# Kernel optimization log

Measured on AMD Instinct MI355X. Metric: run time of the kernel, lower is better.

## Reference

```python
import jax, jax.numpy as jnp
import numpy as np

B, T, C = 2, 2048, 2048
N_HEAD, N_KV_HEAD = 16, 4
HEAD_DIM = C // N_HEAD  # 128
N_REP = N_HEAD // N_KV_HEAD  # 4


def setup_inputs() -> dict:
    key = jax.random.key(0)
    ks = jax.random.split(key, 5)
    x = jax.random.normal(ks[0], (B, T, C), dtype=jnp.float32)
    # RoPE freqs (theta=10000), real cos/sin form of torch's complex freqs_cis
    inv_freq = 1.0 / (10000.0 ** (jnp.arange(0, HEAD_DIM, 2, dtype=jnp.float32) / HEAD_DIM))
    angles = jnp.arange(T, dtype=jnp.float32)[:, None] * inv_freq[None, :]  # [T, HEAD_DIM//2]
    freqs_cos = jnp.cos(angles)
    freqs_sin = jnp.sin(angles)
    s = 0.02
    wq = jax.random.normal(ks[1], (C, C), dtype=jnp.float32) * s
    wk = jax.random.normal(ks[2], (N_KV_HEAD * HEAD_DIM, C), dtype=jnp.float32) * s
    wv = jax.random.normal(ks[3], (N_KV_HEAD * HEAD_DIM, C), dtype=jnp.float32) * s
    wo = jax.random.normal(ks[4], (C, C), dtype=jnp.float32) * s
    return {"x": x, "freqs_cos": freqs_cos, "freqs_sin": freqs_sin,
            "wq": wq, "wk": wk, "wv": wv, "wo": wo}


def _apply_rotary(t, cos, sin):
    # t: [B, T, H, D]; pairs (even, odd) treated as complex, multiplied by cos+i*sin
    tr = t.reshape(*t.shape[:-1], -1, 2)  # [B,T,H,D/2,2]
    t0, t1 = tr[..., 0], tr[..., 1]
    c = cos[None, :, None, :]  # [1,T,1,D/2]
    s = sin[None, :, None, :]
    out = jnp.stack([t0 * c - t1 * s, t0 * s + t1 * c], axis=-1)
    return out.reshape(t.shape)


def reference(x, freqs_cos, freqs_sin, wq, wk, wv, wo):
    b, t, _ = x.shape
    xq = (x @ wq.T).reshape(b, t, N_HEAD, HEAD_DIM)
    xk = (x @ wk.T).reshape(b, t, N_KV_HEAD, HEAD_DIM)
    xv = (x @ wv.T).reshape(b, t, N_KV_HEAD, HEAD_DIM)
    xq = _apply_rotary(xq, freqs_cos, freqs_sin)
    xk = _apply_rotary(xk, freqs_cos, freqs_sin)
    # GQA: repeat_interleave kv heads to n_head
    xk_r = jnp.repeat(xk, N_REP, axis=2)
    xv_r = jnp.repeat(xv, N_REP, axis=2)
    # [B,H,T,D]
    q = xq.transpose(0, 2, 1, 3)
    k = xk_r.transpose(0, 2, 1, 3)
    v = xv_r.transpose(0, 2, 1, 3)
    scale = 1.0 / jnp.sqrt(jnp.float32(HEAD_DIM))
    scores = jnp.einsum('bhtd,bhsd->bhts', q, k) * scale
    causal = jnp.tril(jnp.ones((t, t), dtype=bool))
    scores = jnp.where(causal[None, None], scores, jnp.finfo(scores.dtype).min)
    attn = jax.nn.softmax(scores, axis=-1)
    y = jnp.einsum('bhts,bhsd->bhtd', attn, v)
    y = y.transpose(0, 2, 1, 3).reshape(b, t, C)
    return y @ wo.T
```

## Files before the change

### kernel.cpp

```cpp
#include <hip/hip_runtime.h>

typedef __attribute__((ext_vector_type(8))) __bf16 bf16x8;
typedef __attribute__((ext_vector_type(4))) __bf16 bf16x4;
typedef __attribute__((ext_vector_type(4))) float floatx4;

#define MFMA16x16x32 __builtin_amdgcn_mfma_f32_16x16x32_bf16

__device__ __forceinline__ void async_load16(const void* g, void* l) {
  __builtin_amdgcn_global_load_lds((const __attribute__((address_space(1))) void*)g,
                                   (__attribute__((address_space(3))) void*)l, 16, 0, 0);
}

__global__ __launch_bounds__(256) void cast_all_kernel(const float* __restrict__ x,
                                                       const float* __restrict__ wq,
                                                       const float* __restrict__ wk,
                                                       const float* __restrict__ wv,
                                                       const float* __restrict__ wo,
                                                       __bf16* __restrict__ dst) {
  int i = blockIdx.x * blockDim.x + threadIdx.x;
  const float* src;
  int off;
  if (i < 2097152)      { src = x;  off = 0; }
  else if (i < 3145728) { src = wq; off = 2097152; }
  else if (i < 3407872) { src = wk; off = 3145728; }
  else if (i < 3670016) { src = wv; off = 3407872; }
  else                  { src = wo; off = 3670016; }
  float4 v = ((const float4*)src)[i - off];
  bf16x4 o;
  o[0] = (__bf16)v.x; o[1] = (__bf16)v.y; o[2] = (__bf16)v.z; o[3] = (__bf16)v.w;
  *(bf16x4*)(dst + (size_t)i * 4) = o;
}

template <int MODE>
__global__ __launch_bounds__(256, 3) void gemm_bt(const __bf16* __restrict__ A,
                                                  const __bf16* __restrict__ Bw,
                                                  float* __restrict__ C,
                                                  const float* __restrict__ cs,
                                                  const float* __restrict__ sn,
                                                  __bf16* __restrict__ qb,
                                                  __bf16* __restrict__ kb,
                                                  __bf16* __restrict__ vtg,
                                                  int M, int N, int K) {
  __shared__ __bf16 As[128][64];
  __shared__ __bf16 Bs[128][64];
  const int tid = threadIdx.x;
  const int wave = tid >> 6, lane = tid & 63;
  const int quad = lane >> 4, l16 = lane & 15;
  const int wm = (wave >> 1) * 64, wn = (wave & 1) * 64;
  const int row0 = blockIdx.y * 128, col0 = blockIdx.x * 128;
  const int lr = lane >> 3, ls = lane & 7;
  const int segg = ls ^ lr;
  floatx4 acc[4][4] = {};
  const __bf16* Ab = A + (size_t)row0 * K + segg * 8;
  const __bf16* Bb = Bw + (size_t)col0 * K + segg * 8;
  for (int k0 = 0; k0 < K; k0 += 64) {
    __syncthreads();
#pragma unroll
    for (int i = 0; i < 4; i++) {
      int c = wave * 4 + i;
      int r = c * 8 + lr;
      async_load16(Ab + (size_t)r * K + k0, &As[c * 8][0]);
      async_load16(Bb + (size_t)r * K + k0, &Bs[c * 8][0]);
    }
    __syncthreads();
#pragma unroll
    for (int kk = 0; kk < 64; kk += 32) {
      bf16x8 af[4], bfr[4];
#pragma unroll
      for (int mt = 0; mt < 4; mt++) {
        int row = wm + mt * 16 + l16;
        int seg = ((kk >> 3) + quad) ^ (row & 7);
        af[mt] = *(const bf16x8*)&As[row][seg * 8];
      }
#pragma unroll
      for (int nt = 0; nt < 4; nt++) {
        int row = wn + nt * 16 + l16;
        int seg = ((kk >> 3) + quad) ^ (row & 7);
        bfr[nt] = *(const bf16x8*)&Bs[row][seg * 8];
      }
#pragma unroll
      for (int mt = 0; mt < 4; mt++)
#pragma unroll
        for (int nt = 0; nt < 4; nt++)
          acc[mt][nt] = MFMA16x16x32(af[mt], bfr[nt], acc[mt][nt], 0, 0, 0);
    }
  }
  if (MODE == 0) {
#pragma unroll
    for (int mt = 0; mt < 4; mt++)
#pragma unroll
      for (int nt = 0; nt < 4; nt++)
#pragma unroll
        for (int r = 0; r < 4; r++) {
          int row = row0 + wm + mt * 16 + quad * 4 + r;
          int col = col0 + wn + nt * 16 + l16;
          C[(size_t)row * N + col] = acc[mt][nt][r];
        }
  } else {
#pragma unroll
    for (int mt = 0; mt < 4; mt++)
#pragma unroll
      for (int nt = 0; nt < 4; nt++) {
        const int cbase = col0 + wn + nt * 16;
        const int c = cbase + l16;
#pragma unroll
        for (int r = 0; r < 4; r++) {
          int row = row0 + wm + mt * 16 + quad * 4 + r;
          int t = row & 2047;
          float v = acc[mt][nt][r];
          float vp = __shfl_xor(v, 1);
          if (cbase < 2048) {
            int i = (c & 127) >> 1;
            float co = cs[t * 64 + i], si = sn[t * 64 + i];
            qb[(size_t)row * 2048 + c] =
                (__bf16)((v * co + ((c & 1) ? vp : -vp) * si) * 0.1275411391f);
          } else if (cbase < 2560) {
            int i = (c & 127) >> 1;
            float co = cs[t * 64 + i], si = sn[t * 64 + i];
            kb[(size_t)row * 512 + c - 2048] = (__bf16)(v * co + ((c & 1) ? vp : -vp) * si);
          } else {
            int vd = c - 2560;
            vtg[((size_t)(row >> 11) * 512 + vd) * 2048 + t] = (__bf16)v;
          }
        }
      }
  }
}

__global__ __launch_bounds__(256, 2) void attn_kernel(const __bf16* __restrict__ qb,
                                                      const __bf16* __restrict__ kb,
                                                      const __bf16* __restrict__ vtg,
                                                      __bf16* __restrict__ yb) {
  const int id = blockIdx.x;
  const int q1 = id >> 8;
  const int cc = id & 255;
  const int kvh = cc & 3;
  const int b = (cc >> 2) & 1;
  const int s5 = (cc >> 3) & 31;
  const int tile = q1 ? (63 - s5) : s5;
  const int tid = threadIdx.x, wave = tid >> 6, lane = tid & 63;
  const int h = kvh * 4 + wave;
  const int quad = lane >> 4, l16 = lane & 15;
  const int q0 = tile * 32;
  __shared__ __bf16 Ks[2][64][128];
  __shared__ __bf16 Vt[2][128][64];
  __shared__ __bf16 Ps[4][2][16][64];
  const __bf16* kbase = kb + (size_t)b * 2048 * 512 + kvh * 128;
  const __bf16* vbase = vtg + ((size_t)b * 512 + kvh * 128) * 2048;

  const int u16   = (quad ^ (l16 & 3)) * 16;
  const int b2_64 = (l16 & 4) ? 64 : 0;
  char* const ksb = (char*)Ks;
  char* const vtb = (char*)Vt;
  char* const psb = (char*)Ps + wave * 4096;
  char* const kA0 = ksb + l16 * 256 + u16 + b2_64;
  char* const kB0 = kA0 + 64 - 2 * b2_64;
  char* const kA1 = kA0 + 16384;
  char* const kB1 = kB0 + 16384;
  char* const vA0 = vtb + l16 * 128 + u16 + b2_64;
  char* const vB0 = vA0 + 64 - 2 * b2_64;
  char* const vA1 = vA0 + 16384;
  char* const vB1 = vB0 + 16384;
  char* const prA = psb + l16 * 128 + u16 + b2_64;
  char* const prB = prA + 64 - 2 * b2_64;
  const int h16 = (l16 & 8) ? 16 : 0;
  const int q64 = (quad & 1) * 64;
  char* const pw00 = psb + quad * 512 + (l16 & 7) * 2 + h16 + q64;
  char* const pw10 = psb + quad * 512 + (l16 & 7) * 2 + (16 - h16) + q64;
  char* const pw01 = pw00 + 64 - 2 * q64;
  char* const pw11 = pw10 + 64 - 2 * q64;

  const int klr4 = lane >> 4, kls = lane & 15;
  const int vlr8 = lane >> 3, vls = lane & 7;
  const __bf16* ksrc[4];
  const __bf16* vsrc[4];
#pragma unroll
  for (int i = 0; i < 4; i++) {
    int row = (wave * 4 + i) * 4 + klr4;
    ksrc[i] = kbase + (size_t)row * 512 + (kls ^ (row & 7)) * 8;
    int d = (wave * 4 + i) * 8 + vlr8;
    vsrc[i] = vbase + (size_t)d * 2048 + (vls ^ (d & 7)) * 8;
  }
  char* const kdst = ksb + wave * 4096;
  char* const vdst = vtb + wave * 4096;

  auto stage = [&](int pb, int s0) {
#pragma unroll
    for (int i = 0; i < 4; i++)
      async_load16(ksrc[i] + (size_t)s0 * 512, kdst + pb * 16384 + i * 1024);
#pragma unroll
    for (int i = 0; i < 4; i++)
      async_load16(vsrc[i] + s0, vdst + pb * 16384 + i * 1024);
  };

  bf16x8 qf[2][4];
#pragma unroll
  for (int mt = 0; mt < 2; mt++)
#pragma unroll
    for (int kc = 0; kc < 4; kc++)
      qf[mt][kc] = *(const bf16x8*)(qb + (size_t)(b * 2048 + q0 + mt * 16 + l16) * 2048 +
                                    h * 128 + kc * 32 + quad * 8);
  bf16x8 ones;
#pragma unroll
  for (int j = 0; j < 8; j++) ones[j] = (__bf16)1.0f;
  floatx4 o[2][8] = {};
  floatx4 lsum[2] = {};
  const int nblocks = (tile + 2) >> 1;

  stage(0, 0);
  __syncthreads();

  for (int it = 0; it < nblocks; it++) {
    const int cur = it & 1;
    const int s0 = it * 64;
    if (it + 1 < nblocks) stage(cur ^ 1, s0 + 64);
    const char* kA = cur ? kA1 : kA0;
    const char* kB = cur ? kB1 : kB0;
    const char* vA = cur ? vA1 : vA0;
    const char* vB = cur ? vB1 : vB0;
    floatx4 sacc[2][4] = {};
    __builtin_amdgcn_s_setprio(1);
#pragma unroll
    for (int kc = 0; kc < 4; kc++) {
      const char* kbp = (kc & 1) ? kB : kA;
      bf16x8 bfr[4];
#pragma unroll
      for (int nt = 0; nt < 4; nt++)
        bfr[nt] = *(const bf16x8*)(kbp + nt * 4096 + (kc >> 1) * 128);
#pragma unroll
      for (int mt = 0; mt < 2; mt++)
#pragma unroll
        for (int nt = 0; nt < 4; nt++)
          sacc[mt][nt] = MFMA16x16x32(qf[mt][kc], bfr[nt], sacc[mt][nt], 0, 0, 0);
    }
    __builtin_amdgcn_s_setprio(0);
    const bool diag = (it == nblocks - 1);
#pragma unroll
    for (int mt = 0; mt < 2; mt++)
#pragma unroll
      for (int r = 0; r < 4; r++) {
        const int qg = q0 + mt * 16 + quad * 4 + r;
#pragma unroll
        for (int nt = 0; nt < 4; nt++) {
          float p = __builtin_exp2f(sacc[mt][nt][r]);
          if (diag) { int keyg = s0 + nt * 16 + l16; p = (keyg <= qg) ? p : 0.f; }
          char* w = (r & 1) ? ((nt < 2) ? pw10 : pw11) : ((nt < 2) ? pw00 : pw01);
          *(__bf16*)(w + mt * 2048 + r * 128 + ((nt & 1) ^ (r >> 1)) * 32) = (__bf16)p;
        }
      }
    __builtin_amdgcn_s_setprio(1);
#pragma unroll
    for (int c2 = 0; c2 < 2; c2++) {
      const char* pr = c2 ? prB : prA;
      const char* vv = c2 ? vB : vA;
      bf16x8 pa[2];
#pragma unroll
      for (int mt = 0; mt < 2; mt++) {
        pa[mt] = *(const bf16x8*)(pr + mt * 2048);
        lsum[mt] = MFMA16x16x32(pa[mt], ones, lsum[mt], 0, 0, 0);
      }
#pragma unroll
      for (int dt = 0; dt < 8; dt++) {
        bf16x8 vf = *(const bf16x8*)(vv + dt * 2048);
#pragma unroll
        for (int mt = 0; mt < 2; mt++)
          o[mt][dt] = MFMA16x16x32(pa[mt], vf, o[mt][dt], 0, 0, 0);
      }
    }
    __builtin_amdgcn_s_setprio(0);
    __syncthreads();
  }
#pragma unroll
  for (int mt = 0; mt < 2; mt++) {
    float inv[4];
#pragma unroll
    for (int r = 0; r < 4; r++) inv[r] = 1.f / lsum[mt][r];
#pragma unroll
    for (int dt = 0; dt < 8; dt++)
#pragma unroll
      for (int r = 0; r < 4; r++) {
        int qg = q0 + mt * 16 + quad * 4 + r;
        yb[(size_t)(b * 2048 + qg) * 2048 + h * 128 + dt * 16 + l16] =
            (__bf16)(o[mt][dt][r] * inv[r]);
      }
  }
}

extern "C" void kernel_launch(void* const* d_in, const int* in_sizes, int n_in,
                              void* d_out, int out_size, void* d_ws, size_t ws_size,
                              hipStream_t stream) {
  const float* x  = (const float*)d_in[0];
  const float* fc = (const float*)d_in[1];
  const float* fs = (const float*)d_in[2];
  const float* wq = (const float*)d_in[3];
  const float* wk = (const float*)d_in[4];
  const float* wv = (const float*)d_in[5];
  const float* wo = (const float*)d_in[6];
  float* out = (float*)d_out;
  char* ws = (char*)d_ws;

  __bf16* xb   = (__bf16*)(ws);
  __bf16* wqkv = (__bf16*)(ws + 16777216);
  __bf16* wob  = (__bf16*)(ws + 29360128);
  __bf16* qbuf = (__bf16*)(ws + 37748736);
  __bf16* kbuf = (__bf16*)(ws + 54525952);
  __bf16* vtg  = (__bf16*)(ws + 58720256);
  __bf16* ybuf = (__bf16*)(ws + 62914560);

  cast_all_kernel<<<18432, 256, 0, stream>>>(x, wq, wk, wv, wo, xb);

  gemm_bt<1><<<dim3(24, 32), 256, 0, stream>>>(xb, wqkv, nullptr, fc, fs,
                                               qbuf, kbuf, vtg, 4096, 3072, 2048);

  attn_kernel<<<dim3(512), 256, 0, stream>>>(qbuf, kbuf, vtg, ybuf);

  gemm_bt<0><<<dim3(16, 32), 256, 0, stream>>>(ybuf, wob, out, nullptr, nullptr,
                                               nullptr, nullptr, nullptr, 4096, 2048, 2048);
}
```

Before: 304.2 us.

## Split long causal attention tiles across two blocks and stage V-transpose through LDS

```diff
diff --git a/kernel.cpp b/kernel.cpp
--- a/kernel.cpp
+++ b/kernel.cpp
@@ -102,49 +102,77 @@
 #pragma unroll
       for (int nt = 0; nt < 4; nt++) {
         const int cbase = col0 + wn + nt * 16;
-        const int c = cbase + l16;
-#pragma unroll
-        for (int r = 0; r < 4; r++) {
-          int row = row0 + wm + mt * 16 + quad * 4 + r;
-          int t = row & 2047;
-          float v = acc[mt][nt][r];
-          float vp = __shfl_xor(v, 1);
-          if (cbase < 2048) {
+        if (cbase < 2560) {
+          const int c = cbase + l16;
+#pragma unroll
+          for (int r = 0; r < 4; r++) {
+            int row = row0 + wm + mt * 16 + quad * 4 + r;
+            int t = row & 2047;
+            float v = acc[mt][nt][r];
+            float vp = __shfl_xor(v, 1);
             int i = (c & 127) >> 1;
             float co = cs[t * 64 + i], si = sn[t * 64 + i];
-            qb[(size_t)row * 2048 + c] =
-                (__bf16)((v * co + ((c & 1) ? vp : -vp) * si) * 0.1275411391f);
-          } else if (cbase < 2560) {
-            int i = (c & 127) >> 1;
-            float co = cs[t * 64 + i], si = sn[t * 64 + i];
-            kb[(size_t)row * 512 + c - 2048] = (__bf16)(v * co + ((c & 1) ? vp : -vp) * si);
-          } else {
-            int vd = c - 2560;
-            vtg[((size_t)(row >> 11) * 512 + vd) * 2048 + t] = (__bf16)v;
+            float rv = v * co + ((c & 1) ? vp : -vp) * si;
+            if (cbase < 2048) {
+              qb[(size_t)row * 2048 + c] = (__bf16)(rv * 0.1275411391f);
+            } else {
+              kb[(size_t)row * 512 + c - 2048] = (__bf16)rv;
+            }
           }
         }
       }
+    __syncthreads();
+    __bf16* Vl = &As[0][0] + wave * 1024;
+    const int brow = row0 + wm;
+#pragma unroll
+    for (int nt = 0; nt < 4; nt++) {
+      const int cbase = col0 + wn + nt * 16;
+      if (cbase >= 2560) {
+#pragma unroll
+        for (int mt = 0; mt < 4; mt++)
+#pragma unroll
+          for (int r = 0; r < 4; r++)
+            Vl[l16 * 64 + mt * 16 + quad * 4 + r] = (__bf16)acc[mt][nt][r];
+        asm volatile("" ::: "memory");
+        const int vB = cbase - 2560;
+#pragma unroll
+        for (int p = 0; p < 4; p++) {
+          int vdl = p * 4 + (lane >> 4);
+          int tl = (lane & 15) * 4;
+          bf16x4 val = *(const bf16x4*)&Vl[vdl * 64 + tl];
+          *(bf16x4*)&vtg[((size_t)(brow >> 11) * 512 + vB + vdl) * 2048 +
+                         (brow & 2047) + tl] = val;
+        }
+        asm volatile("" ::: "memory");
+      }
+    }
   }
 }
 
 __global__ __launch_bounds__(256, 2) void attn_kernel(const __bf16* __restrict__ qb,
                                                       const __bf16* __restrict__ kb,
                                                       const __bf16* __restrict__ vtg,
-                                                      __bf16* __restrict__ yb) {
+                                                      __bf16* __restrict__ yb,
+                                                      float* __restrict__ opart,
+                                                      float* __restrict__ lpart,
+                                                      int* __restrict__ ctr,
+                                                      int* __restrict__ ready) {
   const int id = blockIdx.x;
-  const int q1 = id >> 8;
-  const int cc = id & 255;
-  const int kvh = cc & 3;
-  const int b = (cc >> 2) & 1;
-  const int s5 = (cc >> 3) & 31;
-  const int tile = q1 ? (63 - s5) : s5;
+  int grp, tile, chunk, split;
+  if (id < 512) { grp = id >> 6; tile = 32 + ((id & 63) >> 1); chunk = id & 1; split = 1; }
+  else          { int k = id - 512; grp = k >> 5; tile = k & 31; chunk = 0; split = 0; }
+  const int kvh = grp & 3, b = grp >> 2;
   const int tid = threadIdx.x, wave = tid >> 6, lane = tid & 63;
   const int h = kvh * 4 + wave;
   const int quad = lane >> 4, l16 = lane & 15;
   const int q0 = tile * 32;
+  const int nb = (tile + 2) >> 1;
+  const int it0 = chunk * 16;
+  const int it1 = split ? (chunk ? nb : 16) : nb;
   __shared__ __bf16 Ks[2][64][128];
   __shared__ __bf16 Vt[2][128][64];
   __shared__ __bf16 Ps[4][2][16][64];
+  __shared__ int tk_sh;
   const __bf16* kbase = kb + (size_t)b * 2048 * 512 + kvh * 128;
   const __bf16* vbase = vtg + ((size_t)b * 512 + kvh * 128) * 2048;
 
@@ -205,15 +233,14 @@
   for (int j = 0; j < 8; j++) ones[j] = (__bf16)1.0f;
   floatx4 o[2][8] = {};
   floatx4 lsum[2] = {};
-  const int nblocks = (tile + 2) >> 1;
-
-  stage(0, 0);
+
+  stage(it0 & 1, it0 * 64);
   __syncthreads();
 
-  for (int it = 0; it < nblocks; it++) {
+  for (int it = it0; it < it1; it++) {
     const int cur = it & 1;
     const int s0 = it * 64;
-    if (it + 1 < nblocks) stage(cur ^ 1, s0 + 64);
+    if (it + 1 < it1) stage(cur ^ 1, s0 + 64);
     const char* kA = cur ? kA1 : kA0;
     const char* kB = cur ? kB1 : kB0;
     const char* vA = cur ? vA1 : vA0;
@@ -234,7 +261,7 @@
           sacc[mt][nt] = MFMA16x16x32(qf[mt][kc], bfr[nt], sacc[mt][nt], 0, 0, 0);
     }
     __builtin_amdgcn_s_setprio(0);
-    const bool diag = (it == nblocks - 1);
+    const bool diag = (it == nb - 1);
 #pragma unroll
     for (int mt = 0; mt < 2; mt++)
 #pragma unroll
@@ -270,19 +297,86 @@
     __builtin_amdgcn_s_setprio(0);
     __syncthreads();
   }
-#pragma unroll
-  for (int mt = 0; mt < 2; mt++) {
-    float inv[4];
-#pragma unroll
-    for (int r = 0; r < 4; r++) inv[r] = 1.f / lsum[mt][r];
-#pragma unroll
-    for (int dt = 0; dt < 8; dt++)
-#pragma unroll
-      for (int r = 0; r < 4; r++) {
-        int qg = q0 + mt * 16 + quad * 4 + r;
-        yb[(size_t)(b * 2048 + qg) * 2048 + h * 128 + dt * 16 + l16] =
-            (__bf16)(o[mt][dt][r] * inv[r]);
-      }
+
+  if (!split) {
+#pragma unroll
+    for (int mt = 0; mt < 2; mt++) {
+      float inv[4];
+#pragma unroll
+      for (int r = 0; r < 4; r++) inv[r] = 1.f / lsum[mt][r];
+#pragma unroll
+      for (int dt = 0; dt < 8; dt++)
+#pragma unroll
+        for (int r = 0; r < 4; r++) {
+          int qg = q0 + mt * 16 + quad * 4 + r;
+          yb[(size_t)(b * 2048 + qg) * 2048 + h * 128 + dt * 16 + l16] =
+              (__bf16)(o[mt][dt][r] * inv[r]);
+        }
+    }
+  } else {
+    const int pair = grp * 32 + (tile - 32);
+    float* oslot = opart + (size_t)pair * 16384;
+    float* lslot = lpart + (size_t)pair * 128;
+    if (tid == 0)
+      tk_sh = __hip_atomic_fetch_add(&ctr[pair], 1, __ATOMIC_RELAXED,
+                                     __HIP_MEMORY_SCOPE_AGENT);
+    __syncthreads();
+    const int tk = tk_sh;
+    if (tk == 0) {
+#pragma unroll
+      for (int mt = 0; mt < 2; mt++)
+#pragma unroll
+        for (int dt = 0; dt < 8; dt++)
+          *(floatx4*)&oslot[(((wave * 2 + mt) * 8 + dt) << 8) + lane * 4] = o[mt][dt];
+      if (l16 == 0) {
+#pragma unroll
+        for (int mt = 0; mt < 2; mt++)
+#pragma unroll
+          for (int r = 0; r < 4; r++)
+            lslot[wave * 32 + mt * 16 + quad * 4 + r] = lsum[mt][r];
+      }
+      __threadfence();
+      __syncthreads();
+      if (tid == 0)
+        __hip_atomic_store(&ready[pair], 1, __ATOMIC_RELEASE, __HIP_MEMORY_SCOPE_AGENT);
+    } else {
+      if (tid == 0) {
+        while (__hip_atomic_load(&ready[pair], __ATOMIC_ACQUIRE,
+                                 __HIP_MEMORY_SCOPE_AGENT) == 0)
+          __builtin_amdgcn_s_sleep(8);
+      }
+      __syncthreads();
+      __threadfence();
+#pragma unroll
+      for (int mt = 0; mt < 2; mt++) {
+#pragma unroll
+        for (int dt = 0; dt < 8; dt++) {
+          const float* po = &oslot[(((wave * 2 + mt) * 8 + dt) << 8) + lane * 4];
+#pragma unroll
+          for (int c = 0; c < 4; c++)
+            o[mt][dt][c] += __hip_atomic_load(po + c, __ATOMIC_RELAXED,
+                                              __HIP_MEMORY_SCOPE_AGENT);
+        }
+#pragma unroll
+        for (int r = 0; r < 4; r++)
+          lsum[mt][r] += __hip_atomic_load(&lslot[wave * 32 + mt * 16 + quad * 4 + r],
+                                           __ATOMIC_RELAXED, __HIP_MEMORY_SCOPE_AGENT);
+      }
+#pragma unroll
+      for (int mt = 0; mt < 2; mt++) {
+        float inv[4];
+#pragma unroll
+        for (int r = 0; r < 4; r++) inv[r] = 1.f / lsum[mt][r];
+#pragma unroll
+        for (int dt = 0; dt < 8; dt++)
+#pragma unroll
+          for (int r = 0; r < 4; r++) {
+            int qg = q0 + mt * 16 + quad * 4 + r;
+            yb[(size_t)(b * 2048 + qg) * 2048 + h * 128 + dt * 16 + l16] =
+                (__bf16)(o[mt][dt][r] * inv[r]);
+          }
+      }
+    }
   }
 }
 
@@ -307,12 +401,20 @@
   __bf16* vtg  = (__bf16*)(ws + 58720256);
   __bf16* ybuf = (__bf16*)(ws + 62914560);
 
+  float* opart = (float*)ws;
+  int*   ctr   = (int*)(ws + 16777216);
+  int*   rdy   = (int*)(ws + 16777216 + 1024);
+  float* lpart = (float*)(ws + 16777216 + 4096);
+
   cast_all_kernel<<<18432, 256, 0, stream>>>(x, wq, wk, wv, wo, xb);
 
   gemm_bt<1><<<dim3(24, 32), 256, 0, stream>>>(xb, wqkv, nullptr, fc, fs,
                                                qbuf, kbuf, vtg, 4096, 3072, 2048);
 
-  attn_kernel<<<dim3(512), 256, 0, stream>>>(qbuf, kbuf, vtg, ybuf);
+  hipMemsetAsync(ctr, 0, 2048, stream);
+
+  attn_kernel<<<dim3(768), 256, 0, stream>>>(qbuf, kbuf, vtg, ybuf,
+                                             opart, lpart, ctr, rdy);
 
   gemm_bt<0><<<dim3(16, 32), 256, 0, stream>>>(ybuf, wob, out, nullptr, nullptr,
                                                nullptr, nullptr, nullptr, 4096, 2048, 2048);
```

Result: slower. 422.1 us (+38.7%).

## Stage V-transpose stores through LDS and use partial vmcnt waits in attention

Applied to the files above, without the earlier changes.

```diff
diff --git a/kernel.cpp b/kernel.cpp
--- a/kernel.cpp
+++ b/kernel.cpp
@@ -102,28 +102,50 @@
 #pragma unroll
       for (int nt = 0; nt < 4; nt++) {
         const int cbase = col0 + wn + nt * 16;
-        const int c = cbase + l16;
-#pragma unroll
-        for (int r = 0; r < 4; r++) {
-          int row = row0 + wm + mt * 16 + quad * 4 + r;
-          int t = row & 2047;
-          float v = acc[mt][nt][r];
-          float vp = __shfl_xor(v, 1);
-          if (cbase < 2048) {
+        if (cbase < 2560) {
+          const int c = cbase + l16;
+#pragma unroll
+          for (int r = 0; r < 4; r++) {
+            int row = row0 + wm + mt * 16 + quad * 4 + r;
+            int t = row & 2047;
+            float v = acc[mt][nt][r];
+            float vp = __shfl_xor(v, 1);
             int i = (c & 127) >> 1;
             float co = cs[t * 64 + i], si = sn[t * 64 + i];
-            qb[(size_t)row * 2048 + c] =
-                (__bf16)((v * co + ((c & 1) ? vp : -vp) * si) * 0.1275411391f);
-          } else if (cbase < 2560) {
-            int i = (c & 127) >> 1;
-            float co = cs[t * 64 + i], si = sn[t * 64 + i];
-            kb[(size_t)row * 512 + c - 2048] = (__bf16)(v * co + ((c & 1) ? vp : -vp) * si);
-          } else {
-            int vd = c - 2560;
-            vtg[((size_t)(row >> 11) * 512 + vd) * 2048 + t] = (__bf16)v;
+            float rv = v * co + ((c & 1) ? vp : -vp) * si;
+            if (cbase < 2048) {
+              qb[(size_t)row * 2048 + c] = (__bf16)(rv * 0.1275411391f);
+            } else {
+              kb[(size_t)row * 512 + c - 2048] = (__bf16)rv;
+            }
           }
         }
       }
+    __syncthreads();
+    __bf16* Vl = &As[0][0] + wave * 1024;
+    const int brow = row0 + wm;
+#pragma unroll
+    for (int nt = 0; nt < 4; nt++) {
+      const int cbase = col0 + wn + nt * 16;
+      if (cbase >= 2560) {
+#pragma unroll
+        for (int mt = 0; mt < 4; mt++)
+#pragma unroll
+          for (int r = 0; r < 4; r++)
+            Vl[l16 * 64 + mt * 16 + quad * 4 + r] = (__bf16)acc[mt][nt][r];
+        asm volatile("" ::: "memory");
+        const int vB = cbase - 2560;
+#pragma unroll
+        for (int p = 0; p < 4; p++) {
+          int vdl = p * 4 + (lane >> 4);
+          int tl = (lane & 15) * 4;
+          bf16x4 val = *(const bf16x4*)&Vl[vdl * 64 + tl];
+          *(bf16x4*)&vtg[((size_t)(brow >> 11) * 512 + vB + vdl) * 2048 +
+                         (brow & 2047) + tl] = val;
+        }
+        asm volatile("" ::: "memory");
+      }
+    }
   }
 }
 
@@ -208,12 +230,18 @@
   const int nblocks = (tile + 2) >> 1;
 
   stage(0, 0);
-  __syncthreads();
 
   for (int it = 0; it < nblocks; it++) {
     const int cur = it & 1;
     const int s0 = it * 64;
-    if (it + 1 < nblocks) stage(cur ^ 1, s0 + 64);
+    asm volatile("s_barrier" ::: "memory");
+    if (it + 1 < nblocks) {
+      stage(cur ^ 1, s0 + 64);
+      asm volatile("s_waitcnt vmcnt(8)" ::: "memory");
+    } else {
+      asm volatile("s_waitcnt vmcnt(0)" ::: "memory");
+    }
+    asm volatile("s_barrier" ::: "memory");
     const char* kA = cur ? kA1 : kA0;
     const char* kB = cur ? kB1 : kB0;
     const char* vA = cur ? vA1 : vA0;
@@ -268,7 +296,6 @@
       }
     }
     __builtin_amdgcn_s_setprio(0);
-    __syncthreads();
   }
 #pragma unroll
   for (int mt = 0; mt < 2; mt++) {
```

After: 307.6 us. No clear change (+1.1%).
